# Kernel tuning notes

Hardware: AMD Instinct MI355X
Metric: run time of the kernel (lower is better)

## Reference

```python
import jax, jax.numpy as jnp
import numpy as np

B, N, D, H, V, L = 32, 64, 128, 256, 32000, 3  # batch, nodes, embd_dim, msg_hid, vocab, num_layers


def _linear_init(key, fan_in, fan_out):
    k1, k2 = jax.random.split(key)
    s = 1.0 / np.sqrt(fan_in)
    W = jax.random.uniform(k1, (fan_out, fan_in), jnp.float32, -s, s)
    b = jax.random.uniform(k2, (fan_out,), jnp.float32, -s, s)
    return W, b


def setup_inputs() -> dict:
    key = jax.random.key(0)
    ks = jax.random.split(key, 7)
    x = jax.random.randint(ks[0], (B, N), 0, V)                      # token ids
    arcs = jax.random.randint(ks[1], (B, N, N), 0, 2).astype(jnp.int32)
    lengths = jnp.ones((B, N), dtype=jnp.int32)                      # unused by forward
    embd_table = jax.random.normal(ks[2], (V, D), jnp.float32)
    embd_table = embd_table.at[0].set(0.0)                           # padding_idx = 0
    W1_0, b1_0 = _linear_init(ks[3], 2 * D, H)
    W2_0, b2_0 = _linear_init(ks[4], H, D)
    W1_1, b1_1 = _linear_init(ks[5], 2 * D, H)
    W2_1, b2_1 = _linear_init(ks[6], H, D)
    return dict(x=x, arcs=arcs, lengths=lengths, embd_table=embd_table,
                W1_0=W1_0, b1_0=b1_0, W2_0=W2_0, b2_0=b2_0,
                W1_1=W1_1, b1_1=b1_1, W2_1=W2_1, b2_1=b2_1)


def reference(x, arcs, lengths, embd_table,
              W1_0, b1_0, W2_0, b2_0, W1_1, b1_1, W2_1, b2_1):
    # Edge k = (row=k//n, col=k%n). Caller passes senders_idxs=one_hot(cols),
    # receivers_idxs=one_hot(rows); aggregation sums messages over rows.
    # Equivalent gather/scatter expressed as (B,n,n,·) broadcast + sum over axis 2.
    b, n = x.shape
    d = embd_table.shape[1]
    E = embd_table[x]                                   # (B,n,d)
    a = arcs.astype(E.dtype)[..., None]                 # (B,n,n,1) edge-type-1 weight

    def mlp(pre, W1, b1, W2, b2):
        h = jax.nn.relu(jnp.einsum('brce,he->brch', pre, W1) + b1)
        return jax.nn.relu(jnp.einsum('brch,dh->brcd', h, W2) + b2)

    for _ in range(L):
        senders = jnp.broadcast_to(E[:, None, :, :], (b, n, n, d))    # col embedding
        receivers = jnp.broadcast_to(E[:, :, None, :], (b, n, n, d))  # row embedding
        pre = jnp.concatenate([senders, receivers], axis=-1)          # (B,n,n,2d)
        m0 = mlp(pre, W1_0, b1_0, W2_0, b2_0)
        m1 = mlp(pre, W1_1, b1_1, W2_1, b2_1)
        all_msgs = m0 * (1.0 - a) + m1 * a                            # (B,n,n,d)
        agg = all_msgs.sum(axis=2)                                    # scatter-add over rows
        E = E + agg
    return E[:, 0, :]
```

## Files before the change

kernel.cpp:

```cpp
#include <hip/hip_runtime.h>
#include <hip/hip_bf16.h>
#include <stdint.h>


#define NB 32
#define NN 64
#define DD 128
#define HH 256

typedef __attribute__((ext_vector_type(4))) float f32x4;
typedef __attribute__((ext_vector_type(8))) _Float16 f16x8;

__device__ __forceinline__ uint64_t cvt4h(f32x4 v) {
  union { _Float16 h[4]; uint64_t u; } x;
  x.h[0] = (_Float16)v[0]; x.h[1] = (_Float16)v[1];
  x.h[2] = (_Float16)v[2]; x.h[3] = (_Float16)v[3];
  return x.u;
}

__global__ __launch_bounds__(256) void k_setup(const int* __restrict__ x,
                                               const float* __restrict__ table,
                                               float* __restrict__ E0,
                                               const float* __restrict__ W1_0,
                                               const float* __restrict__ W1_1,
                                               const float* __restrict__ W2_0,
                                               const float* __restrict__ W2_1,
                                               _Float16* __restrict__ W1fp,
                                               _Float16* __restrict__ W2fp) {
  int bid = blockIdx.x, t = threadIdx.x;
  if (bid < 256) {
    int i = bid * 256 + t;
    int node = i >> 5;
    ((f32x4*)E0)[i] = ((const f32x4*)table)[(size_t)x[node] * 32 + (i & 31)];
  } else {
    int tid = (bid - 256) * 256 + t;
    const float* src; uint64_t* dst; int off;
    if (tid < 32768) {
      src = (tid < 16384) ? W1_0 : W1_1;
      off = tid & 16383;
      dst = (uint64_t*)W1fp + (tid >> 14) * 16384 + off;
    } else {
      int t2 = tid - 32768;
      src = (t2 < 8192) ? W2_0 : W2_1;
      off = t2 & 8191;
      dst = (uint64_t*)W2fp + (t2 >> 13) * 8192 + off;
    }
    *dst = cvt4h(((const f32x4*)src)[off]);
  }
}

template <int NSP, int NR>
__global__ __launch_bounds__(256) void k_fused(
    const float* __restrict__ E0,
    const float* __restrict__ spA,
    const float* __restrict__ spB,
    float* __restrict__ spOut,
    const _Float16* __restrict__ W1fp,
    const _Float16* __restrict__ W2fp,
    const float* __restrict__ b1_0, const float* __restrict__ b1_1,
    const float* __restrict__ b2_0, const float* __restrict__ b2_1,
    const int* __restrict__ arcs) {
  __shared__ char lds[53248];
  char* Els = lds;
  char* Tsl = lds + 16384;
  char* Trl = lds + 49152;

  int t = threadIdx.x;
  int rg = blockIdx.x, b = blockIdx.y, p = blockIdx.z;
  int rbase = rg * 8;
  int lane = t & 63, w = t >> 6, col = lane & 15, khi = lane >> 4;
  const f32x4 z4 = {0.f, 0.f, 0.f, 0.f};

  {
    const f32x4* e0 = (const f32x4*)(E0 + (size_t)b * NN * DD);
    const f32x4* a0 = (const f32x4*)(spA + (size_t)b * NN * DD);
    const f32x4* a1 = (const f32x4*)(spA + (size_t)(NB + b) * NN * DD);
    const f32x4* c0 = (const f32x4*)(spB + (size_t)b * NN * DD);
    const f32x4* c1 = (const f32x4*)(spB + (size_t)(NB + b) * NN * DD);
#pragma unroll
    for (int ii = 0; ii < 8; ++ii) {
      int idx = ii * 256 + t;
      f32x4 v = e0[idx];
      if (NSP >= 1) v += a0[idx] + a1[idx];
      if (NSP >= 2) v += c0[idx] + c1[idx];
      int node = idx >> 5, ck = idx & 31;
      *(uint64_t*)(Els + node * 256 + ((ck * 8) ^ ((node & 7) << 4))) = cvt4h(v);
    }
  }
  __syncthreads();

  const _Float16* Wq = W1fp + p * 65536;
  const float* b1p = p ? b1_1 : b1_0;
  int eswz = (col & 7) << 4;

#pragma unroll
  for (int nth = 0; nth < 2; ++nth) {
    f16x8 bfr[2][4];
#pragma unroll
    for (int nt = 0; nt < 2; ++nt) {
      int h = w * 64 + nth * 32 + nt * 16 + col;
#pragma unroll
      for (int ks = 0; ks < 4; ++ks)
        bfr[nt][ks] = *(const f16x8*)(Wq + h * 256 + ks * 32 + khi * 8);
    }
    f32x4 tacc[4][2];
#pragma unroll
    for (int mt = 0; mt < 4; ++mt) { tacc[mt][0] = z4; tacc[mt][1] = z4; }
#pragma unroll
    for (int ks = 0; ks < 4; ++ks) {
      f16x8 a[4];
#pragma unroll
      for (int mt = 0; mt < 4; ++mt)
        a[mt] = *(const f16x8*)(Els + (mt * 16 + col) * 256 +
                                ((ks * 64 + khi * 16) ^ eswz));
#pragma unroll
      for (int mt = 0; mt < 4; ++mt) {
        tacc[mt][0] = __builtin_amdgcn_mfma_f32_16x16x32_f16(a[mt], bfr[0][ks],
                                                             tacc[mt][0], 0, 0, 0);
        tacc[mt][1] = __builtin_amdgcn_mfma_f32_16x16x32_f16(a[mt], bfr[1][ks],
                                                             tacc[mt][1], 0, 0, 0);
      }
    }
#pragma unroll
    for (int mt = 0; mt < 4; ++mt)
#pragma unroll
      for (int nt = 0; nt < 2; ++nt) {
        int h = w * 64 + nth * 32 + nt * 16 + col;
#pragma unroll
        for (int j = 0; j < 4; ++j) {
          int c = mt * 16 + khi * 4 + j;
          *(_Float16*)(Tsl + c * 512 + ((h * 2) ^ ((c & 7) << 4))) =
              (_Float16)tacc[mt][nt][j];
        }
      }
  }
  {
    int mt_t = (NR == 1) ? 0 : (rg >> 1);
    int sel = (NR == 1) ? 0 : (rg & 1);
#pragma unroll
    for (int nth = 0; nth < 2; ++nth) {
      f16x8 bfr[2][4];
#pragma unroll
      for (int nt = 0; nt < 2; ++nt) {
        int h = w * 64 + nth * 32 + nt * 16 + col;
#pragma unroll
        for (int ks = 0; ks < 4; ++ks)
          bfr[nt][ks] = *(const f16x8*)(Wq + h * 256 + 128 + ks * 32 + khi * 8);
      }
      f32x4 tacc[2] = {z4, z4};
#pragma unroll
      for (int ks = 0; ks < 4; ++ks) {
        f16x8 a = *(const f16x8*)(Els + (mt_t * 16 + col) * 256 +
                                  ((ks * 64 + khi * 16) ^ eswz));
        tacc[0] = __builtin_amdgcn_mfma_f32_16x16x32_f16(a, bfr[0][ks], tacc[0], 0, 0, 0);
        tacc[1] = __builtin_amdgcn_mfma_f32_16x16x32_f16(a, bfr[1][ks], tacc[1], 0, 0, 0);
      }
      if ((khi >> 1) == sel) {
#pragma unroll
        for (int nt = 0; nt < 2; ++nt) {
          int h = w * 64 + nth * 32 + nt * 16 + col;
          float bb = b1p[h];
#pragma unroll
          for (int j = 0; j < 4; ++j) {
            int lr = (khi & 1) * 4 + j;
            *(_Float16*)(Trl + lr * 512 + ((h * 2) ^ ((lr & 7) << 4))) =
                (_Float16)(tacc[nt][j] + bb);
          }
        }
      }
    }
  }
  __syncthreads();

  int d0 = w * 32 + col;
  const _Float16* W2p = W2fp + p * 32768;
  f16x8 bv[2][8];
#pragma unroll
  for (int nt = 0; nt < 2; ++nt)
#pragma unroll
    for (int ks = 0; ks < 8; ++ks)
      bv[nt][ks] = *(const f16x8*)(W2p + (d0 + nt * 16) * 256 + ks * 32 + khi * 8);
  const float* b2p = p ? b2_1 : b2_0;
  float b2v[2] = {b2p[d0], b2p[d0 + 16]};
  const char* tsb = Tsl + col * 512;

#pragma unroll 1
  for (int r = 0; r < NR; ++r) {
    asm volatile("" : "+v"(bv[0][0]), "+v"(bv[0][1]), "+v"(bv[0][2]), "+v"(bv[0][3]),
                      "+v"(bv[0][4]), "+v"(bv[0][5]), "+v"(bv[0][6]), "+v"(bv[0][7]),
                      "+v"(bv[1][0]), "+v"(bv[1][1]), "+v"(bv[1][2]), "+v"(bv[1][3]),
                      "+v"(bv[1][4]), "+v"(bv[1][5]), "+v"(bv[1][6]), "+v"(bv[1][7]));
    f32x4 acc[4][2];
#pragma unroll
    for (int mt = 0; mt < 4; ++mt) { acc[mt][0] = z4; acc[mt][1] = z4; }
#pragma unroll
    for (int ks = 0; ks < 8; ++ks) {
      f16x8 trv = *(const f16x8*)(Trl + r * 512 +
                                  ((ks * 64 + khi * 16) ^ ((r & 7) << 4)));
#pragma unroll
      for (int mt = 0; mt < 4; ++mt) {
        f16x8 ts = *(const f16x8*)(tsb + mt * 8192 + ((ks * 64 + khi * 16) ^ eswz));
        f16x8 zv = {};
        f16x8 a = __builtin_elementwise_max(ts + trv, zv);
        acc[mt][0] = __builtin_amdgcn_mfma_f32_16x16x32_f16(a, bv[0][ks],
                                                            acc[mt][0], 0, 0, 0);
        acc[mt][1] = __builtin_amdgcn_mfma_f32_16x16x32_f16(a, bv[1][ks],
                                                            acc[mt][1], 0, 0, 0);
      }
    }
    int rr = rbase + r;
    const int* arow = arcs + ((size_t)(b * NN + rr)) * NN;
    float s0 = 0.f, s1 = 0.f;
#pragma unroll
    for (int mt = 0; mt < 4; ++mt) {
      const int4 av = *(const int4*)(arow + mt * 16 + khi * 4);
#pragma unroll
      for (int j = 0; j < 4; ++j) {
        int ai = (j == 0) ? av.x : (j == 1) ? av.y : (j == 2) ? av.z : av.w;
        float wgt = p ? (float)ai : 1.0f - (float)ai;
        s0 = fmaf(wgt, fmaxf(acc[mt][0][j] + b2v[0], 0.f), s0);
        s1 = fmaf(wgt, fmaxf(acc[mt][1][j] + b2v[1], 0.f), s1);
      }
    }
    s0 += __shfl_xor(s0, 16); s0 += __shfl_xor(s0, 32);
    s1 += __shfl_xor(s1, 16); s1 += __shfl_xor(s1, 32);
    if (khi == 0) {
      if (NR == 1) {
        float* o = spOut + (size_t)(p * NB + b) * DD;
        o[d0] = s0; o[d0 + 16] = s1;
      } else {
        float* o = spOut + ((size_t)(p * NB + b) * NN + rr) * DD;
        o[d0] = s0; o[d0 + 16] = s1;
      }
    }
  }
}

__global__ __launch_bounds__(256) void k_out(const float* __restrict__ E0,
                                             const float* __restrict__ spA,
                                             const float* __restrict__ spB,
                                             const float* __restrict__ spC,
                                             float* __restrict__ out) {
  int i = blockIdx.x * 256 + threadIdx.x;
  int b = i >> 7, d = i & 127;
  float acc = E0[(size_t)b * NN * DD + d];
  acc += spA[(size_t)b * NN * DD + d] + spA[(size_t)(NB + b) * NN * DD + d];
  acc += spB[(size_t)b * NN * DD + d] + spB[(size_t)(NB + b) * NN * DD + d];
  acc += spC[(size_t)b * DD + d] + spC[(size_t)(NB + b) * DD + d];
  out[i] = acc;
}

extern "C" void kernel_launch(void* const* d_in, const int* in_sizes, int n_in,
                              void* d_out, int out_size, void* d_ws, size_t ws_size,
                              hipStream_t stream) {
  const int* x       = (const int*)d_in[0];
  const int* arcs    = (const int*)d_in[1];
  const float* table = (const float*)d_in[3];
  const float* W1_0  = (const float*)d_in[4];
  const float* b1_0  = (const float*)d_in[5];
  const float* W2_0  = (const float*)d_in[6];
  const float* b2_0  = (const float*)d_in[7];
  const float* W1_1  = (const float*)d_in[8];
  const float* b1_1  = (const float*)d_in[9];
  const float* W2_1  = (const float*)d_in[10];
  const float* b2_1  = (const float*)d_in[11];
  float* out = (float*)d_out;

  char* ws = (char*)d_ws;
  float* E0        = (float*)ws;
  _Float16* W1fp   = (_Float16*)(ws + (1u << 20));
  _Float16* W2fp   = (_Float16*)(ws + (1u << 20) + (256u << 10));
  float* SpA       = (float*)(ws + (2u << 20));
  float* SpB       = (float*)(ws + (4u << 20));
  float* SpC       = (float*)(ws + (6u << 20));

  k_setup<<<448, 256, 0, stream>>>(x, table, E0, W1_0, W1_1, W2_0, W2_1,
                                   W1fp, W2fp);
  k_fused<0, 8><<<dim3(8, 32, 2), 256, 0, stream>>>(
      E0, E0, E0, SpA, W1fp, W2fp, b1_0, b1_1, b2_0, b2_1, arcs);
  k_fused<1, 8><<<dim3(8, 32, 2), 256, 0, stream>>>(
      E0, SpA, E0, SpB, W1fp, W2fp, b1_0, b1_1, b2_0, b2_1, arcs);
  k_fused<2, 1><<<dim3(1, 32, 2), 256, 0, stream>>>(
      E0, SpA, SpB, SpC, W1fp, W2fp, b1_0, b1_1, b2_0, b2_1, arcs);
  k_out<<<16, 256, 0, stream>>>(E0, SpA, SpB, SpC, out);
}
```

Baseline: 102.1 us.

## Swap first-layer GEMM operands, alias LDS, and halve rows per block

The first MLP GEMM is restructured so W1 is the A operand and node embeddings are the B operand. Sender and receiver projections are computed in one combined loop, and results are stored as packed 4-wide fp16 writes. The Tsl buffer now reuses the Els region after a barrier, which cuts LDS to 36 KB. Rows per block drop from 8 to 4, doubling the grid for the first two layers. The aim is more occupancy and parallelism and fewer scalar LDS stores, at the cost of recomputing the sender projection in twice as many blocks.

```diff
diff --git a/kernel.cpp b/kernel.cpp
--- a/kernel.cpp
+++ b/kernel.cpp
@@ -60,14 +60,14 @@
     const float* __restrict__ b1_0, const float* __restrict__ b1_1,
     const float* __restrict__ b2_0, const float* __restrict__ b2_1,
     const int* __restrict__ arcs) {
-  __shared__ char lds[53248];
+  __shared__ char lds[36864];
   char* Els = lds;
-  char* Tsl = lds + 16384;
-  char* Trl = lds + 49152;
+  char* Tsl = lds;
+  char* Trl = lds + 32768;
 
   int t = threadIdx.x;
   int rg = blockIdx.x, b = blockIdx.y, p = blockIdx.z;
-  int rbase = rg * 8;
+  int rbase = rg * NR;
   int lane = t & 63, w = t >> 6, col = lane & 15, khi = lane >> 4;
   const f32x4 z4 = {0.f, 0.f, 0.f, 0.f};
 
@@ -91,83 +91,57 @@
 
   const _Float16* Wq = W1fp + p * 65536;
   const float* b1p = p ? b1_1 : b1_0;
-  int eswz = (col & 7) << 4;
-
-#pragma unroll
-  for (int nth = 0; nth < 2; ++nth) {
-    f16x8 bfr[2][4];
-#pragma unroll
-    for (int nt = 0; nt < 2; ++nt) {
-      int h = w * 64 + nth * 32 + nt * 16 + col;
-#pragma unroll
-      for (int ks = 0; ks < 4; ++ks)
-        bfr[nt][ks] = *(const f16x8*)(Wq + h * 256 + ks * 32 + khi * 8);
-    }
-    f32x4 tacc[4][2];
-#pragma unroll
-    for (int mt = 0; mt < 4; ++mt) { tacc[mt][0] = z4; tacc[mt][1] = z4; }
-#pragma unroll
-    for (int ks = 0; ks < 4; ++ks) {
-      f16x8 a[4];
-#pragma unroll
-      for (int mt = 0; mt < 4; ++mt)
-        a[mt] = *(const f16x8*)(Els + (mt * 16 + col) * 256 +
-                                ((ks * 64 + khi * 16) ^ eswz));
-#pragma unroll
-      for (int mt = 0; mt < 4; ++mt) {
-        tacc[mt][0] = __builtin_amdgcn_mfma_f32_16x16x32_f16(a[mt], bfr[0][ks],
-                                                             tacc[mt][0], 0, 0, 0);
-        tacc[mt][1] = __builtin_amdgcn_mfma_f32_16x16x32_f16(a[mt], bfr[1][ks],
-                                                             tacc[mt][1], 0, 0, 0);
-      }
-    }
-#pragma unroll
-    for (int mt = 0; mt < 4; ++mt)
-#pragma unroll
-      for (int nt = 0; nt < 2; ++nt) {
-        int h = w * 64 + nth * 32 + nt * 16 + col;
-#pragma unroll
-        for (int j = 0; j < 4; ++j) {
-          int c = mt * 16 + khi * 4 + j;
-          *(_Float16*)(Tsl + c * 512 + ((h * 2) ^ ((c & 7) << 4))) =
-              (_Float16)tacc[mt][nt][j];
-        }
-      }
-  }
-  {
-    int mt_t = (NR == 1) ? 0 : (rg >> 1);
-    int sel = (NR == 1) ? 0 : (rg & 1);
-#pragma unroll
-    for (int nth = 0; nth < 2; ++nth) {
-      f16x8 bfr[2][4];
-#pragma unroll
-      for (int nt = 0; nt < 2; ++nt) {
-        int h = w * 64 + nth * 32 + nt * 16 + col;
-#pragma unroll
-        for (int ks = 0; ks < 4; ++ks)
-          bfr[nt][ks] = *(const f16x8*)(Wq + h * 256 + 128 + ks * 32 + khi * 8);
-      }
-      f32x4 tacc[2] = {z4, z4};
-#pragma unroll
-      for (int ks = 0; ks < 4; ++ks) {
-        f16x8 a = *(const f16x8*)(Els + (mt_t * 16 + col) * 256 +
-                                  ((ks * 64 + khi * 16) ^ eswz));
-        tacc[0] = __builtin_amdgcn_mfma_f32_16x16x32_f16(a, bfr[0][ks], tacc[0], 0, 0, 0);
-        tacc[1] = __builtin_amdgcn_mfma_f32_16x16x32_f16(a, bfr[1][ks], tacc[1], 0, 0, 0);
-      }
-      if ((khi >> 1) == sel) {
-#pragma unroll
-        for (int nt = 0; nt < 2; ++nt) {
-          int h = w * 64 + nth * 32 + nt * 16 + col;
-          float bb = b1p[h];
-#pragma unroll
-          for (int j = 0; j < 4; ++j) {
-            int lr = (khi & 1) * 4 + j;
-            *(_Float16*)(Trl + lr * 512 + ((h * 2) ^ ((lr & 7) << 4))) =
-                (_Float16)(tacc[nt][j] + bb);
-          }
-        }
-      }
+  int g = rbase >> 4, cb = rbase & 15;
+
+  f32x4 taccS[4][4];
+  f32x4 taccR[4];
+#pragma unroll
+  for (int mt = 0; mt < 4; ++mt) {
+#pragma unroll
+    for (int nt = 0; nt < 4; ++nt) taccS[mt][nt] = z4;
+    taccR[mt] = z4;
+  }
+#pragma unroll
+  for (int ks = 0; ks < 4; ++ks) {
+    f16x8 be[4];
+#pragma unroll
+    for (int nt = 0; nt < 4; ++nt) {
+      int c = nt * 16 + col;
+      be[nt] = *(const f16x8*)(Els + c * 256 + ((ks * 64 + khi * 16) ^ ((c & 7) << 4)));
+    }
+    int gc = g * 16 + col;
+    f16x8 beg = *(const f16x8*)(Els + gc * 256 + ((ks * 64 + khi * 16) ^ ((gc & 7) << 4)));
+#pragma unroll
+    for (int mt = 0; mt < 4; ++mt) {
+      int h = w * 64 + mt * 16 + col;
+      f16x8 aw = *(const f16x8*)(Wq + h * 256 + ks * 32 + khi * 8);
+#pragma unroll
+      for (int nt = 0; nt < 4; ++nt)
+        taccS[mt][nt] = __builtin_amdgcn_mfma_f32_16x16x32_f16(aw, be[nt],
+                                                               taccS[mt][nt], 0, 0, 0);
+      f16x8 awr = *(const f16x8*)(Wq + h * 256 + 128 + ks * 32 + khi * 8);
+      taccR[mt] = __builtin_amdgcn_mfma_f32_16x16x32_f16(awr, beg,
+                                                         taccR[mt], 0, 0, 0);
+    }
+  }
+  __syncthreads();
+
+#pragma unroll
+  for (int mt = 0; mt < 4; ++mt) {
+    int h0 = w * 64 + mt * 16 + khi * 4;
+#pragma unroll
+    for (int nt = 0; nt < 4; ++nt) {
+      int c = nt * 16 + col;
+      *(uint64_t*)(Tsl + c * 512 + ((h0 * 2) ^ ((c & 7) << 4))) = cvt4h(taccS[mt][nt]);
+    }
+  }
+  if (col >= cb && col < cb + NR) {
+    int lr = col - cb;
+#pragma unroll
+    for (int mt = 0; mt < 4; ++mt) {
+      int h0 = w * 64 + mt * 16 + khi * 4;
+      f32x4 v = taccR[mt] + *(const f32x4*)(b1p + h0);
+      *(uint64_t*)(Trl + lr * 512 + h0 * 2) = cvt4h(v);
     }
   }
   __syncthreads();
@@ -182,24 +156,20 @@
       bv[nt][ks] = *(const f16x8*)(W2p + (d0 + nt * 16) * 256 + ks * 32 + khi * 8);
   const float* b2p = p ? b2_1 : b2_0;
   float b2v[2] = {b2p[d0], b2p[d0 + 16]};
-  const char* tsb = Tsl + col * 512;
 
 #pragma unroll 1
   for (int r = 0; r < NR; ++r) {
-    asm volatile("" : "+v"(bv[0][0]), "+v"(bv[0][1]), "+v"(bv[0][2]), "+v"(bv[0][3]),
-                      "+v"(bv[0][4]), "+v"(bv[0][5]), "+v"(bv[0][6]), "+v"(bv[0][7]),
-                      "+v"(bv[1][0]), "+v"(bv[1][1]), "+v"(bv[1][2]), "+v"(bv[1][3]),
-                      "+v"(bv[1][4]), "+v"(bv[1][5]), "+v"(bv[1][6]), "+v"(bv[1][7]));
     f32x4 acc[4][2];
 #pragma unroll
     for (int mt = 0; mt < 4; ++mt) { acc[mt][0] = z4; acc[mt][1] = z4; }
 #pragma unroll
     for (int ks = 0; ks < 8; ++ks) {
-      f16x8 trv = *(const f16x8*)(Trl + r * 512 +
-                                  ((ks * 64 + khi * 16) ^ ((r & 7) << 4)));
+      f16x8 trv = *(const f16x8*)(Trl + r * 512 + ks * 64 + khi * 16);
 #pragma unroll
       for (int mt = 0; mt < 4; ++mt) {
-        f16x8 ts = *(const f16x8*)(tsb + mt * 8192 + ((ks * 64 + khi * 16) ^ eswz));
+        int c = mt * 16 + col;
+        f16x8 ts = *(const f16x8*)(Tsl + c * 512 +
+                                   ((ks * 64 + khi * 16) ^ ((c & 7) << 4)));
         f16x8 zv = {};
         f16x8 a = __builtin_elementwise_max(ts + trv, zv);
         acc[mt][0] = __builtin_amdgcn_mfma_f32_16x16x32_f16(a, bv[0][ks],
@@ -276,9 +246,9 @@
 
   k_setup<<<448, 256, 0, stream>>>(x, table, E0, W1_0, W1_1, W2_0, W2_1,
                                    W1fp, W2fp);
-  k_fused<0, 8><<<dim3(8, 32, 2), 256, 0, stream>>>(
+  k_fused<0, 4><<<dim3(16, 32, 2), 256, 0, stream>>>(
       E0, E0, E0, SpA, W1fp, W2fp, b1_0, b1_1, b2_0, b2_1, arcs);
-  k_fused<1, 8><<<dim3(8, 32, 2), 256, 0, stream>>>(
+  k_fused<1, 4><<<dim3(16, 32, 2), 256, 0, stream>>>(
       E0, SpA, E0, SpB, W1fp, W2fp, b1_0, b1_1, b2_0, b2_1, arcs);
   k_fused<2, 1><<<dim3(1, 32, 2), 256, 0, stream>>>(
       E0, SpA, SpB, SpC, W1fp, W2fp, b1_0, b1_1, b2_0, b2_1, arcs);
```

After: 136.7 us. 1.34x slower.

## Double block to 512 threads, split rows across wave halves and merge W1 passes

Applied to the files above, without the earlier changes.

Fused layer kernel now runs 8 waves per block instead of 4. Each wave computes 32 hidden units of the first MLP layer, with sender and receiver projections in a single pass. In the second layer the two halves of the block each take 4 of the 8 rows. The goal is more latency hiding and parallelism in a grid with few blocks, at the cost of more register pressure and an extra barrier.

```diff
diff --git a/kernel.cpp b/kernel.cpp
--- a/kernel.cpp
+++ b/kernel.cpp
@@ -50,7 +50,7 @@
 }
 
 template <int NSP, int NR>
-__global__ __launch_bounds__(256) void k_fused(
+__global__ __launch_bounds__(512) void k_fused(
     const float* __restrict__ E0,
     const float* __restrict__ spA,
     const float* __restrict__ spB,
@@ -65,10 +65,16 @@
   char* Tsl = lds + 16384;
   char* Trl = lds + 49152;
 
+  constexpr int NRW = (NR == 8) ? 4 : 1;
+  constexpr int DNT = (NR == 8) ? 2 : 1;
+
   int t = threadIdx.x;
   int rg = blockIdx.x, b = blockIdx.y, p = blockIdx.z;
-  int rbase = rg * 8;
+  int rbase = rg * NR;
   int lane = t & 63, w = t >> 6, col = lane & 15, khi = lane >> 4;
+  int rh = (NR == 8) ? (w >> 2) : 0;
+  int wl = (NR == 8) ? (w & 3) : w;
+  int d0 = wl * (DNT * 16) + col;
   const f32x4 z4 = {0.f, 0.f, 0.f, 0.f};
 
   {
@@ -78,8 +84,8 @@
     const f32x4* c0 = (const f32x4*)(spB + (size_t)b * NN * DD);
     const f32x4* c1 = (const f32x4*)(spB + (size_t)(NB + b) * NN * DD);
 #pragma unroll
-    for (int ii = 0; ii < 8; ++ii) {
-      int idx = ii * 256 + t;
+    for (int ii = 0; ii < 4; ++ii) {
+      int idx = ii * 512 + t;
       f32x4 v = e0[idx];
       if (NSP >= 1) v += a0[idx] + a1[idx];
       if (NSP >= 2) v += c0[idx] + c1[idx];
@@ -91,126 +97,116 @@
 
   const _Float16* Wq = W1fp + p * 65536;
   const float* b1p = p ? b1_1 : b1_0;
-  int eswz = (col & 7) << 4;
-
-#pragma unroll
-  for (int nth = 0; nth < 2; ++nth) {
-    f16x8 bfr[2][4];
+  int g = (NR == 8) ? (rg >> 1) : 0;
+  int sel = (NR == 8) ? (rg & 1) : 0;
+
+  f32x4 taccS[4][2];
+  f32x4 taccR[2] = {z4, z4};
+#pragma unroll
+  for (int mt = 0; mt < 4; ++mt) { taccS[mt][0] = z4; taccS[mt][1] = z4; }
+  {
+    f16x8 bfr[2][4], bfrR[2][4];
 #pragma unroll
     for (int nt = 0; nt < 2; ++nt) {
-      int h = w * 64 + nth * 32 + nt * 16 + col;
-#pragma unroll
-      for (int ks = 0; ks < 4; ++ks)
-        bfr[nt][ks] = *(const f16x8*)(Wq + h * 256 + ks * 32 + khi * 8);
-    }
-    f32x4 tacc[4][2];
-#pragma unroll
-    for (int mt = 0; mt < 4; ++mt) { tacc[mt][0] = z4; tacc[mt][1] = z4; }
+      int h = w * 32 + nt * 16 + col;
+#pragma unroll
+      for (int ks = 0; ks < 4; ++ks) {
+        bfr[nt][ks]  = *(const f16x8*)(Wq + h * 256 + ks * 32 + khi * 8);
+        bfrR[nt][ks] = *(const f16x8*)(Wq + h * 256 + 128 + ks * 32 + khi * 8);
+      }
+    }
 #pragma unroll
     for (int ks = 0; ks < 4; ++ks) {
       f16x8 a[4];
 #pragma unroll
-      for (int mt = 0; mt < 4; ++mt)
-        a[mt] = *(const f16x8*)(Els + (mt * 16 + col) * 256 +
-                                ((ks * 64 + khi * 16) ^ eswz));
-#pragma unroll
       for (int mt = 0; mt < 4; ++mt) {
-        tacc[mt][0] = __builtin_amdgcn_mfma_f32_16x16x32_f16(a[mt], bfr[0][ks],
-                                                             tacc[mt][0], 0, 0, 0);
-        tacc[mt][1] = __builtin_amdgcn_mfma_f32_16x16x32_f16(a[mt], bfr[1][ks],
-                                                             tacc[mt][1], 0, 0, 0);
-      }
-    }
-#pragma unroll
-    for (int mt = 0; mt < 4; ++mt)
-#pragma unroll
-      for (int nt = 0; nt < 2; ++nt) {
-        int h = w * 64 + nth * 32 + nt * 16 + col;
-#pragma unroll
-        for (int j = 0; j < 4; ++j) {
-          int c = mt * 16 + khi * 4 + j;
-          *(_Float16*)(Tsl + c * 512 + ((h * 2) ^ ((c & 7) << 4))) =
-              (_Float16)tacc[mt][nt][j];
-        }
-      }
-  }
-  {
-    int mt_t = (NR == 1) ? 0 : (rg >> 1);
-    int sel = (NR == 1) ? 0 : (rg & 1);
-#pragma unroll
-    for (int nth = 0; nth < 2; ++nth) {
-      f16x8 bfr[2][4];
-#pragma unroll
-      for (int nt = 0; nt < 2; ++nt) {
-        int h = w * 64 + nth * 32 + nt * 16 + col;
-#pragma unroll
-        for (int ks = 0; ks < 4; ++ks)
-          bfr[nt][ks] = *(const f16x8*)(Wq + h * 256 + 128 + ks * 32 + khi * 8);
-      }
-      f32x4 tacc[2] = {z4, z4};
-#pragma unroll
-      for (int ks = 0; ks < 4; ++ks) {
-        f16x8 a = *(const f16x8*)(Els + (mt_t * 16 + col) * 256 +
-                                  ((ks * 64 + khi * 16) ^ eswz));
-        tacc[0] = __builtin_amdgcn_mfma_f32_16x16x32_f16(a, bfr[0][ks], tacc[0], 0, 0, 0);
-        tacc[1] = __builtin_amdgcn_mfma_f32_16x16x32_f16(a, bfr[1][ks], tacc[1], 0, 0, 0);
-      }
-      if ((khi >> 1) == sel) {
-#pragma unroll
-        for (int nt = 0; nt < 2; ++nt) {
-          int h = w * 64 + nth * 32 + nt * 16 + col;
-          float bb = b1p[h];
-#pragma unroll
-          for (int j = 0; j < 4; ++j) {
-            int lr = (khi & 1) * 4 + j;
-            *(_Float16*)(Trl + lr * 512 + ((h * 2) ^ ((lr & 7) << 4))) =
-                (_Float16)(tacc[nt][j] + bb);
-          }
-        }
-      }
+        int c = mt * 16 + col;
+        a[mt] = *(const f16x8*)(Els + c * 256 + ((ks * 64 + khi * 16) ^ ((c & 7) << 4)));
+      }
+#pragma unroll
+      for (int mt = 0; mt < 4; ++mt) {
+        taccS[mt][0] = __builtin_amdgcn_mfma_f32_16x16x32_f16(a[mt], bfr[0][ks],
+                                                              taccS[mt][0], 0, 0, 0);
+        taccS[mt][1] = __builtin_amdgcn_mfma_f32_16x16x32_f16(a[mt], bfr[1][ks],
+                                                              taccS[mt][1], 0, 0, 0);
+      }
+      taccR[0] = __builtin_amdgcn_mfma_f32_16x16x32_f16(a[g], bfrR[0][ks],
+                                                        taccR[0], 0, 0, 0);
+      taccR[1] = __builtin_amdgcn_mfma_f32_16x16x32_f16(a[g], bfrR[1][ks],
+                                                        taccR[1], 0, 0, 0);
     }
   }
   __syncthreads();
 
-  int d0 = w * 32 + col;
+#pragma unroll
+  for (int mt = 0; mt < 4; ++mt)
+#pragma unroll
+    for (int nt = 0; nt < 2; ++nt) {
+      int h = w * 32 + nt * 16 + col;
+#pragma unroll
+      for (int j = 0; j < 4; ++j) {
+        int c = mt * 16 + khi * 4 + j;
+        *(_Float16*)(Tsl + c * 512 + ((h * 2) ^ ((c & 7) << 4))) =
+            (_Float16)taccS[mt][nt][j];
+      }
+    }
+  if ((khi >> 1) == sel) {
+#pragma unroll
+    for (int nt = 0; nt < 2; ++nt) {
+      int h = w * 32 + nt * 16 + col;
+      float bb = b1p[h];
+#pragma unroll
+      for (int j = 0; j < 4; ++j) {
+        int lr = (khi & 1) * 4 + j;
+        *(_Float16*)(Trl + lr * 512 + ((h * 2) ^ ((lr & 7) << 4))) =
+            (_Float16)(taccR[nt][j] + bb);
+      }
+    }
+  }
+  __syncthreads();
+
   const _Float16* W2p = W2fp + p * 32768;
-  f16x8 bv[2][8];
-#pragma unroll
-  for (int nt = 0; nt < 2; ++nt)
+  f16x8 bv[DNT][8];
+#pragma unroll
+  for (int nt = 0; nt < DNT; ++nt)
 #pragma unroll
     for (int ks = 0; ks < 8; ++ks)
       bv[nt][ks] = *(const f16x8*)(W2p + (d0 + nt * 16) * 256 + ks * 32 + khi * 8);
   const float* b2p = p ? b2_1 : b2_0;
-  float b2v[2] = {b2p[d0], b2p[d0 + 16]};
-  const char* tsb = Tsl + col * 512;
+  float b2v[DNT];
+#pragma unroll
+  for (int nt = 0; nt < DNT; ++nt) b2v[nt] = b2p[d0 + nt * 16];
 
 #pragma unroll 1
-  for (int r = 0; r < NR; ++r) {
-    asm volatile("" : "+v"(bv[0][0]), "+v"(bv[0][1]), "+v"(bv[0][2]), "+v"(bv[0][3]),
-                      "+v"(bv[0][4]), "+v"(bv[0][5]), "+v"(bv[0][6]), "+v"(bv[0][7]),
-                      "+v"(bv[1][0]), "+v"(bv[1][1]), "+v"(bv[1][2]), "+v"(bv[1][3]),
-                      "+v"(bv[1][4]), "+v"(bv[1][5]), "+v"(bv[1][6]), "+v"(bv[1][7]));
-    f32x4 acc[4][2];
-#pragma unroll
-    for (int mt = 0; mt < 4; ++mt) { acc[mt][0] = z4; acc[mt][1] = z4; }
+  for (int r = 0; r < NRW; ++r) {
+    int lrr = rh * 4 + r;
+    f32x4 acc[4][DNT];
+#pragma unroll
+    for (int mt = 0; mt < 4; ++mt)
+#pragma unroll
+      for (int nt = 0; nt < DNT; ++nt) acc[mt][nt] = z4;
 #pragma unroll
     for (int ks = 0; ks < 8; ++ks) {
-      f16x8 trv = *(const f16x8*)(Trl + r * 512 +
-                                  ((ks * 64 + khi * 16) ^ ((r & 7) << 4)));
+      f16x8 trv = *(const f16x8*)(Trl + lrr * 512 +
+                                  ((ks * 64 + khi * 16) ^ ((lrr & 7) << 4)));
 #pragma unroll
       for (int mt = 0; mt < 4; ++mt) {
-        f16x8 ts = *(const f16x8*)(tsb + mt * 8192 + ((ks * 64 + khi * 16) ^ eswz));
+        int c = mt * 16 + col;
+        f16x8 ts = *(const f16x8*)(Tsl + c * 512 +
+                                   ((ks * 64 + khi * 16) ^ ((c & 7) << 4)));
         f16x8 zv = {};
         f16x8 a = __builtin_elementwise_max(ts + trv, zv);
-        acc[mt][0] = __builtin_amdgcn_mfma_f32_16x16x32_f16(a, bv[0][ks],
-                                                            acc[mt][0], 0, 0, 0);
-        acc[mt][1] = __builtin_amdgcn_mfma_f32_16x16x32_f16(a, bv[1][ks],
-                                                            acc[mt][1], 0, 0, 0);
-      }
-    }
-    int rr = rbase + r;
+#pragma unroll
+        for (int nt = 0; nt < DNT; ++nt)
+          acc[mt][nt] = __builtin_amdgcn_mfma_f32_16x16x32_f16(a, bv[nt][ks],
+                                                               acc[mt][nt], 0, 0, 0);
+      }
+    }
+    int rr = rbase + lrr;
     const int* arow = arcs + ((size_t)(b * NN + rr)) * NN;
-    float s0 = 0.f, s1 = 0.f;
+    float s[DNT];
+#pragma unroll
+    for (int nt = 0; nt < DNT; ++nt) s[nt] = 0.f;
 #pragma unroll
     for (int mt = 0; mt < 4; ++mt) {
       const int4 av = *(const int4*)(arow + mt * 16 + khi * 4);
@@ -218,20 +214,22 @@
       for (int j = 0; j < 4; ++j) {
         int ai = (j == 0) ? av.x : (j == 1) ? av.y : (j == 2) ? av.z : av.w;
         float wgt = p ? (float)ai : 1.0f - (float)ai;
-        s0 = fmaf(wgt, fmaxf(acc[mt][0][j] + b2v[0], 0.f), s0);
-        s1 = fmaf(wgt, fmaxf(acc[mt][1][j] + b2v[1], 0.f), s1);
-      }
-    }
-    s0 += __shfl_xor(s0, 16); s0 += __shfl_xor(s0, 32);
-    s1 += __shfl_xor(s1, 16); s1 += __shfl_xor(s1, 32);
+#pragma unroll
+        for (int nt = 0; nt < DNT; ++nt)
+          s[nt] = fmaf(wgt, fmaxf(acc[mt][nt][j] + b2v[nt], 0.f), s[nt]);
+      }
+    }
+#pragma unroll
+    for (int nt = 0; nt < DNT; ++nt) {
+      s[nt] += __shfl_xor(s[nt], 16);
+      s[nt] += __shfl_xor(s[nt], 32);
+    }
     if (khi == 0) {
-      if (NR == 1) {
-        float* o = spOut + (size_t)(p * NB + b) * DD;
-        o[d0] = s0; o[d0 + 16] = s1;
-      } else {
-        float* o = spOut + ((size_t)(p * NB + b) * NN + rr) * DD;
-        o[d0] = s0; o[d0 + 16] = s1;
-      }
+      float* o = (NR == 1)
+          ? spOut + (size_t)(p * NB + b) * DD
+          : spOut + ((size_t)(p * NB + b) * NN + rr) * DD;
+#pragma unroll
+      for (int nt = 0; nt < DNT; ++nt) o[d0 + nt * 16] = s[nt];
     }
   }
 }
@@ -276,11 +274,11 @@
 
   k_setup<<<448, 256, 0, stream>>>(x, table, E0, W1_0, W1_1, W2_0, W2_1,
                                    W1fp, W2fp);
-  k_fused<0, 8><<<dim3(8, 32, 2), 256, 0, stream>>>(
+  k_fused<0, 8><<<dim3(8, 32, 2), 512, 0, stream>>>(
       E0, E0, E0, SpA, W1fp, W2fp, b1_0, b1_1, b2_0, b2_1, arcs);
-  k_fused<1, 8><<<dim3(8, 32, 2), 256, 0, stream>>>(
+  k_fused<1, 8><<<dim3(8, 32, 2), 512, 0, stream>>>(
       E0, SpA, E0, SpB, W1fp, W2fp, b1_0, b1_1, b2_0, b2_1, arcs);
-  k_fused<2, 1><<<dim3(1, 32, 2), 256, 0, stream>>>(
+  k_fused<2, 1><<<dim3(1, 32, 2), 512, 0, stream>>>(
       E0, SpA, SpB, SpC, W1fp, W2fp, b1_0, b1_1, b2_0, b2_1, arcs);
   k_out<<<16, 256, 0, stream>>>(E0, SpA, SpB, SpC, out);
 }
```

New measurement: 202.5 us. +98.3%, slower.

## Split sender columns across blocks to double grid parallelism and shrink LDS

Applied to the files above, without the earlier changes.

Each fused block now handles only half of the 64 sender columns (32), so the grid grows from 2 to 4 slices in z and per-block MFMA work and LDS footprint shrink (53 KB to 32 KB). Partial aggregates are written to four slices and summed in the next layer's load and in the output kernel. The receiver transform is now computed only for the block's own rows instead of a 16-row tile. The aim is more blocks and higher occupancy on a small problem, at the cost of duplicated W1 receiver work, more partial-sum traffic, and extra reads when loading each layer's embeddings.

```diff
diff --git a/kernel.cpp b/kernel.cpp
--- a/kernel.cpp
+++ b/kernel.cpp
@@ -60,38 +60,53 @@
     const float* __restrict__ b1_0, const float* __restrict__ b1_1,
     const float* __restrict__ b2_0, const float* __restrict__ b2_1,
     const int* __restrict__ arcs) {
-  __shared__ char lds[53248];
-  char* Els = lds;
-  char* Tsl = lds + 16384;
-  char* Trl = lds + 49152;
+  __shared__ char lds[32768];
+  char* Els_c = lds;
+  char* Els_r = lds + 8192;
+  char* Tsl   = lds + 12288;
+  char* Trl   = lds + 28672;
 
   int t = threadIdx.x;
-  int rg = blockIdx.x, b = blockIdx.y, p = blockIdx.z;
-  int rbase = rg * 8;
+  int rg = blockIdx.x, b = blockIdx.y;
+  int p = blockIdx.z >> 1, ch = blockIdx.z & 1;
+  int rbase = rg * NR;
   int lane = t & 63, w = t >> 6, col = lane & 15, khi = lane >> 4;
   const f32x4 z4 = {0.f, 0.f, 0.f, 0.f};
 
   {
-    const f32x4* e0 = (const f32x4*)(E0 + (size_t)b * NN * DD);
-    const f32x4* a0 = (const f32x4*)(spA + (size_t)b * NN * DD);
-    const f32x4* a1 = (const f32x4*)(spA + (size_t)(NB + b) * NN * DD);
-    const f32x4* c0 = (const f32x4*)(spB + (size_t)b * NN * DD);
-    const f32x4* c1 = (const f32x4*)(spB + (size_t)(NB + b) * NN * DD);
-#pragma unroll
-    for (int ii = 0; ii < 8; ++ii) {
-      int idx = ii * 256 + t;
-      f32x4 v = e0[idx];
-      if (NSP >= 1) v += a0[idx] + a1[idx];
-      if (NSP >= 2) v += c0[idx] + c1[idx];
-      int node = idx >> 5, ck = idx & 31;
-      *(uint64_t*)(Els + node * 256 + ((ck * 8) ^ ((node & 7) << 4))) = cvt4h(v);
+    const float* eb = E0 + (size_t)b * NN * DD;
+#pragma unroll
+    for (int ii = 0; ii < 6; ++ii) {
+      int chunk = ii * 256 + t;
+      int lrow = chunk >> 5, ck = chunk & 31;
+      int node; char* dst;
+      if (lrow < 32) {
+        node = ch * 32 + lrow;
+        dst = Els_c + lrow * 256;
+      } else {
+        int lr = lrow - 32;
+        int nr = rbase + lr; if (nr > 63) nr = 63;
+        node = nr;
+        dst = Els_r + lr * 256;
+      }
+      f32x4 v = ((const f32x4*)(eb + node * DD))[ck];
+      if (NSP >= 1) {
+#pragma unroll
+        for (int s = 0; s < 4; ++s)
+          v += ((const f32x4*)(spA + ((size_t)(s * NB + b) * NN + node) * DD))[ck];
+      }
+      if (NSP >= 2) {
+#pragma unroll
+        for (int s = 0; s < 4; ++s)
+          v += ((const f32x4*)(spB + ((size_t)(s * NB + b) * NN + node) * DD))[ck];
+      }
+      *(uint64_t*)(dst + ((ck * 8) ^ ((lrow & 7) << 4))) = cvt4h(v);
     }
   }
   __syncthreads();
 
   const _Float16* Wq = W1fp + p * 65536;
   const float* b1p = p ? b1_1 : b1_0;
-  int eswz = (col & 7) << 4;
 
 #pragma unroll
   for (int nth = 0; nth < 2; ++nth) {
@@ -103,18 +118,20 @@
       for (int ks = 0; ks < 4; ++ks)
         bfr[nt][ks] = *(const f16x8*)(Wq + h * 256 + ks * 32 + khi * 8);
     }
-    f32x4 tacc[4][2];
-#pragma unroll
-    for (int mt = 0; mt < 4; ++mt) { tacc[mt][0] = z4; tacc[mt][1] = z4; }
+    f32x4 tacc[2][2];
+#pragma unroll
+    for (int mt = 0; mt < 2; ++mt) { tacc[mt][0] = z4; tacc[mt][1] = z4; }
 #pragma unroll
     for (int ks = 0; ks < 4; ++ks) {
-      f16x8 a[4];
-#pragma unroll
-      for (int mt = 0; mt < 4; ++mt)
-        a[mt] = *(const f16x8*)(Els + (mt * 16 + col) * 256 +
-                                ((ks * 64 + khi * 16) ^ eswz));
-#pragma unroll
-      for (int mt = 0; mt < 4; ++mt) {
+      f16x8 a[2];
+#pragma unroll
+      for (int mt = 0; mt < 2; ++mt) {
+        int c = mt * 16 + col;
+        a[mt] = *(const f16x8*)(Els_c + c * 256 +
+                                ((ks * 64 + khi * 16) ^ ((c & 7) << 4)));
+      }
+#pragma unroll
+      for (int mt = 0; mt < 2; ++mt) {
         tacc[mt][0] = __builtin_amdgcn_mfma_f32_16x16x32_f16(a[mt], bfr[0][ks],
                                                              tacc[mt][0], 0, 0, 0);
         tacc[mt][1] = __builtin_amdgcn_mfma_f32_16x16x32_f16(a[mt], bfr[1][ks],
@@ -122,7 +139,7 @@
       }
     }
 #pragma unroll
-    for (int mt = 0; mt < 4; ++mt)
+    for (int mt = 0; mt < 2; ++mt)
 #pragma unroll
       for (int nt = 0; nt < 2; ++nt) {
         int h = w * 64 + nth * 32 + nt * 16 + col;
@@ -134,38 +151,36 @@
         }
       }
   }
-  {
-    int mt_t = (NR == 1) ? 0 : (rg >> 1);
-    int sel = (NR == 1) ? 0 : (rg & 1);
-#pragma unroll
-    for (int nth = 0; nth < 2; ++nth) {
-      f16x8 bfr[2][4];
+#pragma unroll
+  for (int nth = 0; nth < 2; ++nth) {
+    f16x8 bfrR[2][4];
+#pragma unroll
+    for (int nt = 0; nt < 2; ++nt) {
+      int h = w * 64 + nth * 32 + nt * 16 + col;
+#pragma unroll
+      for (int ks = 0; ks < 4; ++ks)
+        bfrR[nt][ks] = *(const f16x8*)(Wq + h * 256 + 128 + ks * 32 + khi * 8);
+    }
+    f32x4 taccR[2] = {z4, z4};
+#pragma unroll
+    for (int ks = 0; ks < 4; ++ks) {
+      f16x8 ar = *(const f16x8*)(Els_r + col * 256 +
+                                 ((ks * 64 + khi * 16) ^ ((col & 7) << 4)));
+      taccR[0] = __builtin_amdgcn_mfma_f32_16x16x32_f16(ar, bfrR[0][ks],
+                                                        taccR[0], 0, 0, 0);
+      taccR[1] = __builtin_amdgcn_mfma_f32_16x16x32_f16(ar, bfrR[1][ks],
+                                                        taccR[1], 0, 0, 0);
+    }
+    if (khi < 2) {
 #pragma unroll
       for (int nt = 0; nt < 2; ++nt) {
         int h = w * 64 + nth * 32 + nt * 16 + col;
-#pragma unroll
-        for (int ks = 0; ks < 4; ++ks)
-          bfr[nt][ks] = *(const f16x8*)(Wq + h * 256 + 128 + ks * 32 + khi * 8);
-      }
-      f32x4 tacc[2] = {z4, z4};
-#pragma unroll
-      for (int ks = 0; ks < 4; ++ks) {
-        f16x8 a = *(const f16x8*)(Els + (mt_t * 16 + col) * 256 +
-                                  ((ks * 64 + khi * 16) ^ eswz));
-        tacc[0] = __builtin_amdgcn_mfma_f32_16x16x32_f16(a, bfr[0][ks], tacc[0], 0, 0, 0);
-        tacc[1] = __builtin_amdgcn_mfma_f32_16x16x32_f16(a, bfr[1][ks], tacc[1], 0, 0, 0);
-      }
-      if ((khi >> 1) == sel) {
-#pragma unroll
-        for (int nt = 0; nt < 2; ++nt) {
-          int h = w * 64 + nth * 32 + nt * 16 + col;
-          float bb = b1p[h];
-#pragma unroll
-          for (int j = 0; j < 4; ++j) {
-            int lr = (khi & 1) * 4 + j;
-            *(_Float16*)(Trl + lr * 512 + ((h * 2) ^ ((lr & 7) << 4))) =
-                (_Float16)(tacc[nt][j] + bb);
-          }
+        float bb = b1p[h];
+#pragma unroll
+        for (int j = 0; j < 4; ++j) {
+          int lr = khi * 4 + j;
+          *(_Float16*)(Trl + lr * 512 + ((h * 2) ^ ((lr & 7) << 4))) =
+              (_Float16)(taccR[nt][j] + bb);
         }
       }
     }
@@ -182,24 +197,21 @@
       bv[nt][ks] = *(const f16x8*)(W2p + (d0 + nt * 16) * 256 + ks * 32 + khi * 8);
   const float* b2p = p ? b2_1 : b2_0;
   float b2v[2] = {b2p[d0], b2p[d0 + 16]};
-  const char* tsb = Tsl + col * 512;
 
 #pragma unroll 1
   for (int r = 0; r < NR; ++r) {
-    asm volatile("" : "+v"(bv[0][0]), "+v"(bv[0][1]), "+v"(bv[0][2]), "+v"(bv[0][3]),
-                      "+v"(bv[0][4]), "+v"(bv[0][5]), "+v"(bv[0][6]), "+v"(bv[0][7]),
-                      "+v"(bv[1][0]), "+v"(bv[1][1]), "+v"(bv[1][2]), "+v"(bv[1][3]),
-                      "+v"(bv[1][4]), "+v"(bv[1][5]), "+v"(bv[1][6]), "+v"(bv[1][7]));
-    f32x4 acc[4][2];
-#pragma unroll
-    for (int mt = 0; mt < 4; ++mt) { acc[mt][0] = z4; acc[mt][1] = z4; }
+    f32x4 acc[2][2];
+#pragma unroll
+    for (int mt = 0; mt < 2; ++mt) { acc[mt][0] = z4; acc[mt][1] = z4; }
 #pragma unroll
     for (int ks = 0; ks < 8; ++ks) {
       f16x8 trv = *(const f16x8*)(Trl + r * 512 +
                                   ((ks * 64 + khi * 16) ^ ((r & 7) << 4)));
 #pragma unroll
-      for (int mt = 0; mt < 4; ++mt) {
-        f16x8 ts = *(const f16x8*)(tsb + mt * 8192 + ((ks * 64 + khi * 16) ^ eswz));
+      for (int mt = 0; mt < 2; ++mt) {
+        int c = mt * 16 + col;
+        f16x8 ts = *(const f16x8*)(Tsl + c * 512 +
+                                   ((ks * 64 + khi * 16) ^ ((c & 7) << 4)));
         f16x8 zv = {};
         f16x8 a = __builtin_elementwise_max(ts + trv, zv);
         acc[mt][0] = __builtin_amdgcn_mfma_f32_16x16x32_f16(a, bv[0][ks],
@@ -209,10 +221,10 @@
       }
     }
     int rr = rbase + r;
-    const int* arow = arcs + ((size_t)(b * NN + rr)) * NN;
+    const int* arow = arcs + ((size_t)(b * NN + rr)) * NN + ch * 32;
     float s0 = 0.f, s1 = 0.f;
 #pragma unroll
-    for (int mt = 0; mt < 4; ++mt) {
+    for (int mt = 0; mt < 2; ++mt) {
       const int4 av = *(const int4*)(arow + mt * 16 + khi * 4);
 #pragma unroll
       for (int j = 0; j < 4; ++j) {
@@ -225,13 +237,11 @@
     s0 += __shfl_xor(s0, 16); s0 += __shfl_xor(s0, 32);
     s1 += __shfl_xor(s1, 16); s1 += __shfl_xor(s1, 32);
     if (khi == 0) {
-      if (NR == 1) {
-        float* o = spOut + (size_t)(p * NB + b) * DD;
-        o[d0] = s0; o[d0 + 16] = s1;
-      } else {
-        float* o = spOut + ((size_t)(p * NB + b) * NN + rr) * DD;
-        o[d0] = s0; o[d0 + 16] = s1;
-      }
+      int slice = p * 2 + ch;
+      float* o = (NR == 1)
+          ? spOut + (size_t)(slice * NB + b) * DD
+          : spOut + ((size_t)(slice * NB + b) * NN + rr) * DD;
+      o[d0] = s0; o[d0 + 16] = s1;
     }
   }
 }
@@ -244,9 +254,12 @@
   int i = blockIdx.x * 256 + threadIdx.x;
   int b = i >> 7, d = i & 127;
   float acc = E0[(size_t)b * NN * DD + d];
-  acc += spA[(size_t)b * NN * DD + d] + spA[(size_t)(NB + b) * NN * DD + d];
-  acc += spB[(size_t)b * NN * DD + d] + spB[(size_t)(NB + b) * NN * DD + d];
-  acc += spC[(size_t)b * DD + d] + spC[(size_t)(NB + b) * DD + d];
+#pragma unroll
+  for (int s = 0; s < 4; ++s) {
+    acc += spA[(size_t)(s * NB + b) * NN * DD + d];
+    acc += spB[(size_t)(s * NB + b) * NN * DD + d];
+    acc += spC[(size_t)(s * NB + b) * DD + d];
+  }
   out[i] = acc;
 }
 
@@ -271,16 +284,16 @@
   _Float16* W1fp   = (_Float16*)(ws + (1u << 20));
   _Float16* W2fp   = (_Float16*)(ws + (1u << 20) + (256u << 10));
   float* SpA       = (float*)(ws + (2u << 20));
-  float* SpB       = (float*)(ws + (4u << 20));
-  float* SpC       = (float*)(ws + (6u << 20));
+  float* SpB       = (float*)(ws + (6u << 20));
+  float* SpC       = (float*)(ws + (10u << 20));
 
   k_setup<<<448, 256, 0, stream>>>(x, table, E0, W1_0, W1_1, W2_0, W2_1,
                                    W1fp, W2fp);
-  k_fused<0, 8><<<dim3(8, 32, 2), 256, 0, stream>>>(
+  k_fused<0, 8><<<dim3(8, 32, 4), 256, 0, stream>>>(
       E0, E0, E0, SpA, W1fp, W2fp, b1_0, b1_1, b2_0, b2_1, arcs);
-  k_fused<1, 8><<<dim3(8, 32, 2), 256, 0, stream>>>(
+  k_fused<1, 8><<<dim3(8, 32, 4), 256, 0, stream>>>(
       E0, SpA, E0, SpB, W1fp, W2fp, b1_0, b1_1, b2_0, b2_1, arcs);
-  k_fused<2, 1><<<dim3(1, 32, 2), 256, 0, stream>>>(
+  k_fused<2, 1><<<dim3(1, 32, 4), 256, 0, stream>>>(
       E0, SpA, SpB, SpC, W1fp, W2fp, b1_0, b1_1, b2_0, b2_1, arcs);
   k_out<<<16, 256, 0, stream>>>(E0, SpA, SpB, SpC, out);
 }
```

After: 111.4 us. +9.1%, slower.
